# Optimization experiments

Measured on AMD Instinct MI355X. Metric: run time of the kernel, lower is better.

Reference implementation:

```python
import jax, jax.numpy as jnp
import numpy as np

B, T, C = 2, 4096, 1024
H, M, CHUNK = 16, 64, 128
D = C // H
DELTA = 1e-6


def setup_inputs() -> dict:
    key = jax.random.key(0)
    ks = jax.random.split(key, 4)
    x = jax.random.normal(ks[0], (B, T, C), dtype=jnp.float32)
    Wqkv = jax.random.normal(ks[1], (3 * C, C), dtype=jnp.float32) * 0.02
    bqkv = jnp.zeros((3 * C,), dtype=jnp.float32)
    Wout = jax.random.normal(ks[2], (C, C), dtype=jnp.float32) * 0.02
    bout = jnp.zeros((C,), dtype=jnp.float32)
    proj = jax.random.normal(ks[3], (H, D, M), dtype=jnp.float32) / np.sqrt(D)
    return {"x": x, "Wqkv": Wqkv, "bqkv": bqkv, "Wout": Wout, "bout": bout, "proj": proj}


def reference(x, Wqkv, bqkv, Wout, bout, proj):
    b, t, c = x.shape
    qkv = x @ Wqkv.T + bqkv                      # (B,T,3C)
    q, k, v = jnp.split(qkv, 3, axis=-1)
    # (B,T,C) -> (B,H,T,D)
    def to_heads(z):
        return z.reshape(b, t, H, D).transpose(0, 2, 1, 3).astype(jnp.float32)
    q, k, v = to_heads(q), to_heads(k), to_heads(v)

    nch = t // CHUNK
    # (B,H,T,D) -> (nch, B, H, Tc, D)
    def to_chunks(z):
        return z.reshape(b, H, nch, CHUNK, D).transpose(2, 0, 1, 3, 4)
    qc, kc, vc = to_chunks(q), to_chunks(k), to_chunks(v)

    mask = jnp.tril(jnp.ones((CHUNK, CHUNK), dtype=jnp.float32))

    def step(carry, inp):
        kv_state, k_state = carry                 # (B,H,M,D), (B,H,M)
        q_ch, k_ch, v_ch = inp                    # (B,H,Tc,D)
        qp = jax.nn.relu(jnp.einsum('bhtd,hdm->bhtm', q_ch, proj))
        kp = jax.nn.relu(jnp.einsum('bhtd,hdm->bhtm', k_ch, proj))
        ctx_hist = jnp.einsum('bhtm,bhmd->bhtd', qp, kv_state)
        norm_hist = jnp.einsum('bhtm,bhm->bht', qp, k_state)
        aw = jnp.einsum('bhtm,bhsm->bhts', qp, kp) * mask  # causal intra-chunk
        ctx_intra = jnp.einsum('bhts,bhsd->bhtd', aw, v_ch)
        norm_intra = aw.sum(-1)
        out = (ctx_hist + ctx_intra) / (norm_hist + norm_intra + DELTA)[..., None]
        new_kv = kv_state + jnp.einsum('bhtm,bhtd->bhmd', kp, v_ch)
        new_k = k_state + kp.sum(2)
        return (new_kv, new_k), out

    carry0 = (jnp.zeros((b, H, M, D), jnp.float32), jnp.zeros((b, H, M), jnp.float32))
    _, outs = jax.lax.scan(step, carry0, (qc, kc, vc))  # (nch,B,H,Tc,D)
    out = outs.transpose(1, 2, 0, 3, 4).reshape(b, H, t, D)  # (B,H,T,D)
    out = out.transpose(0, 2, 1, 3).reshape(b, t, c)          # (B,T,C)
    return out @ Wout.T + bout
```

## Files before the change

### kernel.cpp

```cpp
#include <hip/hip_runtime.h>
#include <stdint.h>

#define HN 16
#define DH 64
#define MF 64
#define CHK 128
#define NCH 32
#define TSEQ 4096
#define CIN 1024
#define C3 3072

typedef __attribute__((ext_vector_type(8))) short bf16x8;
typedef __attribute__((ext_vector_type(4))) float f32x4;

__device__ __forceinline__ unsigned short f2b(float f){
  union{float f;uint32_t u;} v; v.f=f;
  return (unsigned short)((v.u + 0x7fffu + ((v.u>>16)&1u))>>16);
}

#define MFMA(a,b,c) __builtin_amdgcn_mfma_f32_16x16x32_bf16(a,b,c,0,0,0)

typedef __attribute__((address_space(1))) void gbl_t;
typedef __attribute__((address_space(3))) void lds_t;
__device__ __forceinline__ void gload_lds16(const void* g, void* l){
  __builtin_amdgcn_global_load_lds((const gbl_t*)g, (lds_t*)l, 16, 0, 0);
}

__global__ __launch_bounds__(256) void cvt_kernel(const float* __restrict__ src,
                                                  unsigned short* __restrict__ dst, int n4){
  int i = blockIdx.x*256 + threadIdx.x;
  if (i >= n4) return;
  float4 v = ((const float4*)src)[i];
  uint64_t pk = (uint64_t)f2b(v.x) | ((uint64_t)f2b(v.y)<<16)
              | ((uint64_t)f2b(v.z)<<32) | ((uint64_t)f2b(v.w)<<48);
  *(uint64_t*)(dst + (size_t)i*4) = pk;
}

__global__ __launch_bounds__(256) void projt_kernel(const float* __restrict__ proj,
                                                    unsigned short* __restrict__ projT){
  int i = blockIdx.x*256 + threadIdx.x;
  if (i >= HN*DH*MF) return;
  int h = i>>12, r = i&4095, d = r>>6, m = r&63;
  projT[(h<<12) + (m<<6) + d] = f2b(proj[i]);
}

template<int OUT_BF16>
__global__ __launch_bounds__(256) void gemm_bt_kernel(
    const unsigned short* __restrict__ A, const unsigned short* __restrict__ Bt,
    const float* __restrict__ bias, void* __restrict__ Cout,
    int Mm, int Nn, int Kk)
{
  __shared__ unsigned short sA[128*32];
  __shared__ unsigned short sB[128*32];
  int tid = threadIdx.x;
  int w = tid>>6, l = tid&63, g = l>>4, r16 = l&15;
  int nb = Nn>>7;
  int brow = (blockIdx.x / nb)<<7;
  int bcol = (blockIdx.x % nb)<<7;
  int wr = w>>1, wc = w&1;
  f32x4 acc[4][4];
  #pragma unroll
  for (int m=0;m<4;m++)
    #pragma unroll
    for (int n=0;n<4;n++) acc[m][n] = (f32x4){0.f,0.f,0.f,0.f};

  int srow = tid>>2, scol = (tid&3)<<3;
  const unsigned short* Ag0 = A + (size_t)(brow+srow)*Kk + scol;
  const unsigned short* Bg0 = Bt + (size_t)(bcol+srow)*Kk + scol;
  char* lA = (char*)sA + tid*16;
  char* lB = (char*)sB + tid*16;
  size_t step64 = (size_t)64*Kk;

  for (int kk=0; kk<Kk; kk+=32){
    gload_lds16(Ag0 + kk,          lA);
    gload_lds16(Ag0 + kk + step64, lA + 4096);
    gload_lds16(Bg0 + kk,          lB);
    gload_lds16(Bg0 + kk + step64, lB + 4096);
    asm volatile("s_waitcnt vmcnt(0)" ::: "memory");
    __syncthreads();
    bf16x8 af[4], bfr[4];
    #pragma unroll
    for (int m=0;m<4;m++){
      int row = wr*64 + m*16 + r16;
      af[m] = *(const bf16x8*)((const char*)sA + row*64 + g*16);
    }
    #pragma unroll
    for (int n=0;n<4;n++){
      int row = wc*64 + n*16 + r16;
      bfr[n] = *(const bf16x8*)((const char*)sB + row*64 + g*16);
    }
    #pragma unroll
    for (int m=0;m<4;m++)
      #pragma unroll
      for (int n=0;n<4;n++)
        acc[m][n] = MFMA(af[m], bfr[n], acc[m][n]);
    __syncthreads();
  }
  #pragma unroll
  for (int m=0;m<4;m++){
    #pragma unroll
    for (int n=0;n<4;n++){
      int colg = bcol + wc*64 + n*16 + r16;
      float bv = bias[colg];
      #pragma unroll
      for (int j=0;j<4;j++){
        int rowg = brow + wr*64 + m*16 + g*4 + j;
        float v = acc[m][n][j] + bv;
        if (OUT_BF16) ((unsigned short*)Cout)[(size_t)rowg*Nn + colg] = f2b(v);
        else          ((float*)Cout)[(size_t)rowg*Nn + colg] = v;
      }
    }
  }
}

__global__ __launch_bounds__(256) void chunk_stats_kernel(
    const unsigned short* __restrict__ qkvb,
    const unsigned short* __restrict__ projT,
    float* __restrict__ Sbuf, float* __restrict__ ssum)
{
  __shared__ unsigned short s_pT[64*64];
  __shared__ unsigned short s_kpT[64*128];
  __shared__ unsigned short s_vT[64*128];
  __shared__ float s_part[256];

  int bid = blockIdx.x;
  int ch = bid&31, h = (bid>>5)&15, b = bid>>9;
  int tid = threadIdx.x, w = tid>>6, l = tid&63, g = l>>4, r16 = l&15;
  int rowbase = b*TSEQ + ch*CHK;
  const unsigned short* kg = qkvb + (size_t)rowbase*C3 + CIN   + h*DH;
  const unsigned short* vg = qkvb + (size_t)rowbase*C3 + 2*CIN + h*DH;

  {
    const unsigned short* p = projT + (h<<12);
    for (int i = tid; i < 4096; i += 256){
      int m = i>>6, d = i&63;
      *(unsigned short*)((char*)s_pT + m*128 + (((d*2) ^ ((m&7)<<4)))) = p[i];
    }
  }
  for (int i = tid; i < 1024; i += 256){
    int t = i>>3, d0 = (i&7)<<3;
    bf16x8 vv = *(const bf16x8*)(vg + (size_t)t*C3 + d0);
    #pragma unroll
    for (int j=0;j<8;j++){
      int d = d0+j;
      *(unsigned short*)((char*)s_vT + d*256 + (((t*2) ^ ((d&15)<<4)))) = (unsigned short)vv[j];
    }
  }
  __syncthreads();

  f32x4 kacc[2][4];
  #pragma unroll
  for (int tr=0;tr<2;tr++)
    #pragma unroll
    for (int nc=0;nc<4;nc++) kacc[tr][nc] = (f32x4){0.f,0.f,0.f,0.f};
  #pragma unroll
  for (int ks=0; ks<2; ks++){
    bf16x8 a[2];
    #pragma unroll
    for (int tr=0;tr<2;tr++){
      int t = w*32 + tr*16 + r16;
      a[tr] = *(const bf16x8*)(kg + (size_t)t*C3 + ks*32 + g*8);
    }
    #pragma unroll
    for (int nc=0;nc<4;nc++){
      int m = nc*16 + r16;
      bf16x8 bb = *(const bf16x8*)((const char*)s_pT + m*128 + (((ks*64 + g*16) ^ ((m&7)<<4))));
      #pragma unroll
      for (int tr=0;tr<2;tr++)
        kacc[tr][nc] = MFMA(a[tr], bb, kacc[tr][nc]);
    }
  }
  #pragma unroll
  for (int nc=0;nc<4;nc++){
    float v = 0.f;
    #pragma unroll
    for (int tr=0;tr<2;tr++)
      #pragma unroll
      for (int j=0;j<4;j++){
        float x = kacc[tr][nc][j]; x = x>0.f?x:0.f;
        v += x;
        int t = w*32 + tr*16 + g*4 + j;
        int m = nc*16 + r16;
        *(unsigned short*)((char*)s_kpT + m*256 + (((t*2) ^ ((m&15)<<4)))) = f2b(x);
      }
    v += __shfl_xor(v,16); v += __shfl_xor(v,32);
    if (g==0) s_part[w*64 + nc*16 + r16] = v;
  }
  __syncthreads();

  f32x4 sacc[4];
  #pragma unroll
  for (int dc=0;dc<4;dc++) sacc[dc] = (f32x4){0.f,0.f,0.f,0.f};
  int mrow = w*16 + r16;
  #pragma unroll
  for (int ks=0; ks<4; ks++){
    bf16x8 a = *(const bf16x8*)((const char*)s_kpT + mrow*256 + (((ks*64 + g*16) ^ ((mrow&15)<<4))));
    #pragma unroll
    for (int dc=0; dc<4; dc++){
      int d = dc*16 + r16;
      bf16x8 bb = *(const bf16x8*)((const char*)s_vT + d*256 + (((ks*64 + g*16) ^ ((d&15)<<4))));
      sacc[dc] = MFMA(a, bb, sacc[dc]);
    }
  }
  float* So = Sbuf + ((size_t)((b*HN + h)*NCH + ch))*4096;
  #pragma unroll
  for (int dc=0; dc<4; dc++)
    #pragma unroll
    for (int j=0;j<4;j++)
      So[(w*16 + g*4 + j)*64 + dc*16 + r16] = sacc[dc][j];
  if (tid < 64){
    float v = s_part[tid] + s_part[64+tid] + s_part[128+tid] + s_part[192+tid];
    ssum[((size_t)((b*HN + h)*NCH + ch))*64 + tid] = v;
  }
}

__global__ __launch_bounds__(256) void scan_kernel(
  const float* __restrict__ Sbuf, const float* __restrict__ ssum,
  float* __restrict__ kvstate, float* __restrict__ kstate)
{
  int bh = blockIdx.x, tid = threadIdx.x;
  const float4* Sp = (const float4*)(Sbuf + (size_t)bh*NCH*4096);
  float4* kvp = (float4*)(kvstate + (size_t)bh*NCH*4096);
  float4 acc[4];
  #pragma unroll
  for (int q=0;q<4;q++) acc[q] = make_float4(0.f,0.f,0.f,0.f);
  for (int c2=0; c2<NCH; c2++){
    #pragma unroll
    for (int q=0;q<4;q++){
      int idx = c2*1024 + q*256 + tid;
      float4 s = Sp[idx];
      kvp[idx] = acc[q];
      acc[q].x += s.x; acc[q].y += s.y; acc[q].z += s.z; acc[q].w += s.w;
    }
  }
  if (tid < 64){
    float a = 0.f;
    const float* sp = ssum + (size_t)bh*NCH*64;
    float* kp2 = kstate + (size_t)bh*NCH*64;
    for (int c2=0;c2<NCH;c2++){ kp2[c2*64+tid] = a; a += sp[c2*64+tid]; }
  }
}

__global__ __launch_bounds__(256) void chunk_out_kernel(
    const unsigned short* __restrict__ qkvb,
    const unsigned short* __restrict__ projT,
    const float* __restrict__ kvstate,
    const float* __restrict__ kstate,
    unsigned short* __restrict__ attnb)
{
  __shared__ unsigned short s_qp[128*64];
  __shared__ unsigned short s_kp[128*64];
  __shared__ unsigned short s_vT[64*128];
  __shared__ unsigned short s_pa[64*64];

  int bid = blockIdx.x;
  int ch = bid&31, h=(bid>>5)&15, b=bid>>9;
  int tid=threadIdx.x, w=tid>>6, l=tid&63, g=l>>4, r16=l&15;
  int rowbase = b*TSEQ + ch*CHK;
  const unsigned short* qg = qkvb + (size_t)rowbase*C3 + h*DH;
  const unsigned short* kg = qg + CIN;
  const unsigned short* vg = qg + 2*CIN;
  const float* kvg = kvstate + ((size_t)((b*HN+h)*NCH + ch))*4096;
  const float* ksg = kstate  + ((size_t)((b*HN+h)*NCH + ch))*64;

  {
    const unsigned short* p = projT + (h<<12);
    for (int i = tid; i < 4096; i += 256){
      int m = i>>6, d = i&63;
      *(unsigned short*)((char*)s_pa + m*128 + (((d*2) ^ ((m&7)<<4)))) = p[i];
    }
  }
  for (int i = tid; i < 1024; i += 256){
    int t = i>>3, d0 = (i&7)<<3;
    bf16x8 vv = *(const bf16x8*)(vg + (size_t)t*C3 + d0);
    #pragma unroll
    for (int j=0;j<8;j++){
      int d = d0+j;
      *(unsigned short*)((char*)s_vT + d*256 + (((t*2) ^ ((d&15)<<4)))) = (unsigned short)vv[j];
    }
  }
  __syncthreads();

  f32x4 qacc[2][4];
  #pragma unroll
  for (int tr=0;tr<2;tr++)
    #pragma unroll
    for (int nc=0;nc<4;nc++) qacc[tr][nc] = (f32x4){0.f,0.f,0.f,0.f};
  #pragma unroll
  for (int ks=0; ks<2; ks++){
    bf16x8 a[2];
    #pragma unroll
    for (int tr=0;tr<2;tr++){
      int t = w*32 + tr*16 + r16;
      a[tr] = *(const bf16x8*)(qg + (size_t)t*C3 + ks*32 + g*8);
    }
    #pragma unroll
    for (int nc=0;nc<4;nc++){
      int m = nc*16 + r16;
      bf16x8 bb = *(const bf16x8*)((const char*)s_pa + m*128 + (((ks*64 + g*16) ^ ((m&7)<<4))));
      #pragma unroll
      for (int tr=0;tr<2;tr++)
        qacc[tr][nc] = MFMA(a[tr], bb, qacc[tr][nc]);
    }
  }
  float nh[2][4];
  #pragma unroll
  for (int tr=0;tr<2;tr++)
    #pragma unroll
    for (int j=0;j<4;j++) nh[tr][j] = 0.f;
  #pragma unroll
  for (int nc=0;nc<4;nc++){
    float ksv = ksg[nc*16 + r16];
    #pragma unroll
    for (int tr=0;tr<2;tr++)
      #pragma unroll
      for (int j=0;j<4;j++){
        float x = qacc[tr][nc][j]; x = x>0.f?x:0.f;
        nh[tr][j] += x*ksv;
        int t = w*32 + tr*16 + g*4 + j;
        int m = nc*16 + r16;
        *(unsigned short*)((char*)s_qp + t*128 + (((m*2) ^ ((t&7)<<4)))) = f2b(x);
      }
  }
  f32x4 kacc[2][4];
  #pragma unroll
  for (int tr=0;tr<2;tr++)
    #pragma unroll
    for (int nc=0;nc<4;nc++) kacc[tr][nc] = (f32x4){0.f,0.f,0.f,0.f};
  #pragma unroll
  for (int ks=0; ks<2; ks++){
    bf16x8 a[2];
    #pragma unroll
    for (int tr=0;tr<2;tr++){
      int t = w*32 + tr*16 + r16;
      a[tr] = *(const bf16x8*)(kg + (size_t)t*C3 + ks*32 + g*8);
    }
    #pragma unroll
    for (int nc=0;nc<4;nc++){
      int m = nc*16 + r16;
      bf16x8 bb = *(const bf16x8*)((const char*)s_pa + m*128 + (((ks*64 + g*16) ^ ((m&7)<<4))));
      #pragma unroll
      for (int tr=0;tr<2;tr++)
        kacc[tr][nc] = MFMA(a[tr], bb, kacc[tr][nc]);
    }
  }
  #pragma unroll
  for (int nc=0;nc<4;nc++)
    #pragma unroll
    for (int tr=0;tr<2;tr++)
      #pragma unroll
      for (int j=0;j<4;j++){
        float x = kacc[tr][nc][j]; x = x>0.f?x:0.f;
        int t = w*32 + tr*16 + g*4 + j;
        int m = nc*16 + r16;
        *(unsigned short*)((char*)s_kp + t*128 + (((m*2) ^ ((t&7)<<4)))) = f2b(x);
      }
  __syncthreads();

  f32x4 ctx[2][4];
  float ni[2][4];
  #pragma unroll
  for (int tr=0;tr<2;tr++){
    #pragma unroll
    for (int dc=0;dc<4;dc++) ctx[tr][dc] = (f32x4){0.f,0.f,0.f,0.f};
    #pragma unroll
    for (int j=0;j<4;j++) ni[tr][j] = 0.f;
  }

  for (int sb=0; sb<4; sb++){
    f32x4 aw[2][2];
    #pragma unroll
    for (int tr=0;tr<2;tr++)
      #pragma unroll
      for (int sc=0;sc<2;sc++) aw[tr][sc] = (f32x4){0.f,0.f,0.f,0.f};
    #pragma unroll
    for (int ks=0; ks<2; ks++){
      bf16x8 a[2];
      #pragma unroll
      for (int tr=0;tr<2;tr++){
        int t = w*32 + tr*16 + r16;
        a[tr] = *(const bf16x8*)((const char*)s_qp + t*128 + (((ks*64 + g*16) ^ ((t&7)<<4))));
      }
      #pragma unroll
      for (int sc=0;sc<2;sc++){
        int s = sb*32 + sc*16 + r16;
        bf16x8 bb = *(const bf16x8*)((const char*)s_kp + s*128 + (((ks*64 + g*16) ^ ((s&7)<<4))));
        #pragma unroll
        for (int tr=0;tr<2;tr++)
          aw[tr][sc] = MFMA(a[tr], bb, aw[tr][sc]);
      }
    }
    #pragma unroll
    for (int tr=0;tr<2;tr++)
      #pragma unroll
      for (int sc=0;sc<2;sc++)
        #pragma unroll
        for (int j=0;j<4;j++){
          int t = w*32 + tr*16 + g*4 + j;
          int s = sb*32 + sc*16 + r16;
          float x = (s<=t)? aw[tr][sc][j] : 0.f;
          ni[tr][j] += x;
          int sl = sc*16 + r16;
          *(unsigned short*)((char*)s_pa + t*64 + (((sl*2) ^ ((t&3)<<4)))) = f2b(x);
        }
    __syncthreads();
    #pragma unroll
    for (int tr=0;tr<2;tr++){
      int t = w*32 + tr*16 + r16;
      bf16x8 a2 = *(const bf16x8*)((const char*)s_pa + t*64 + (((g*16) ^ ((t&3)<<4))));
      #pragma unroll
      for (int dc=0;dc<4;dc++){
        int d = dc*16 + r16;
        bf16x8 bb = *(const bf16x8*)((const char*)s_vT + d*256 + (((sb*64 + g*16) ^ ((d&15)<<4))));
        ctx[tr][dc] = MFMA(a2, bb, ctx[tr][dc]);
      }
    }
    __syncthreads();
  }

  #pragma unroll
  for (int ks=0; ks<2; ks++){
    bf16x8 a[2];
    #pragma unroll
    for (int tr=0;tr<2;tr++){
      int t = w*32 + tr*16 + r16;
      a[tr] = *(const bf16x8*)((const char*)s_qp + t*128 + (((ks*64 + g*16) ^ ((t&7)<<4))));
    }
    #pragma unroll
    for (int dc=0;dc<4;dc++){
      bf16x8 bb;
      #pragma unroll
      for (int i=0;i<8;i++)
        bb[i] = (short)f2b(kvg[(ks*32 + g*8 + i)*64 + dc*16 + r16]);
      #pragma unroll
      for (int tr=0;tr<2;tr++)
        ctx[tr][dc] = MFMA(a[tr], bb, ctx[tr][dc]);
    }
  }

  float nrm[2][4];
  #pragma unroll
  for (int tr=0;tr<2;tr++)
    #pragma unroll
    for (int j=0;j<4;j++){
      float v = nh[tr][j] + ni[tr][j];
      v += __shfl_xor(v,1); v += __shfl_xor(v,2);
      v += __shfl_xor(v,4); v += __shfl_xor(v,8);
      nrm[tr][j] = v + 1e-6f;
    }

  #pragma unroll
  for (int tr=0;tr<2;tr++)
    #pragma unroll
    for (int dc=0;dc<4;dc++)
      #pragma unroll
      for (int j=0;j<4;j++){
        int t = w*32 + tr*16 + g*4 + j;
        int d = dc*16 + r16;
        attnb[(size_t)(rowbase + t)*CIN + h*DH + d] = f2b(ctx[tr][dc][j] / nrm[tr][j]);
      }
}

extern "C" void kernel_launch(void* const* d_in, const int* in_sizes, int n_in,
                              void* d_out, int out_size, void* d_ws, size_t ws_size,
                              hipStream_t stream)
{
  const float* x    = (const float*)d_in[0];
  const float* Wqkv = (const float*)d_in[1];
  const float* bqkv = (const float*)d_in[2];
  const float* Wout = (const float*)d_in[3];
  const float* bout = (const float*)d_in[4];
  const float* proj = (const float*)d_in[5];

  char* ws = (char*)d_ws;
  unsigned short* xb     = (unsigned short*)(ws + 0);
  unsigned short* attnb  = (unsigned short*)(ws + 0);
  unsigned short* wqkvb  = (unsigned short*)(ws + 16777216);
  float*          ssum   = (float*)(ws + 16777216);
  float*          kstate = (float*)(ws + 17039360);
  unsigned short* qkvb   = (unsigned short*)(ws + 23068672);
  unsigned short* woutb  = (unsigned short*)(ws + 73400320);
  unsigned short* projTb = (unsigned short*)(ws + 75497472);
  float*          Sbuf   = (float*)(ws + 75628544);
  float*          kvstate= (float*)(ws + 92405760);

  cvt_kernel<<<8192, 256, 0, stream>>>(x, xb, 2097152);
  cvt_kernel<<<3072, 256, 0, stream>>>(Wqkv, wqkvb, 786432);
  cvt_kernel<<<1024, 256, 0, stream>>>(Wout, woutb, 262144);
  projt_kernel<<<256, 256, 0, stream>>>(proj, projTb);

  gemm_bt_kernel<1><<<1536, 256, 0, stream>>>(xb, wqkvb, bqkv, qkvb, 8192, 3072, 1024);

  chunk_stats_kernel<<<1024, 256, 0, stream>>>(qkvb, projTb, Sbuf, ssum);
  scan_kernel<<<32, 256, 0, stream>>>(Sbuf, ssum, kvstate, kstate);
  chunk_out_kernel<<<1024, 256, 0, stream>>>(qkvb, projTb, kvstate, kstate, attnb);

  gemm_bt_kernel<0><<<512, 256, 0, stream>>>(attnb, woutb, bout, d_out, 8192, 1024, 1024);
}
```

Measured before the change: 180.4 us.

## Replace GEMM with 256x256 double-buffered 8-wave pipelined kernel

Swaps the simple 128x128 single-buffer bf16 GEMM for a 256x256-tile, 512-thread kernel. It double-buffers 64-wide K slices in LDS, interleaves global-to-LDS staging across eight MFMA sub-phases, uses an XOR swizzle to avoid bank conflicts, raises wave priority around MFMA bursts, and remaps workgroups across XCDs. The goal is to hide global-load latency and improve data reuse in both projection GEMMs. In exchange it uses much more LDS per block, has fewer blocks (128 for the output GEMM, which may underfill the GPU), and needs careful vmcnt accounting, including wrap-around prefetches past the end of K.

New measurement: 191.8 us. 6.3% more time.

```diff
diff --git a/kernel.cpp b/kernel.cpp
--- a/kernel.cpp
+++ b/kernel.cpp
@@ -44,70 +44,132 @@
   projT[(h<<12) + (m<<6) + d] = f2b(proj[i]);
 }
 
-template<int OUT_BF16>
-__global__ __launch_bounds__(256) void gemm_bt_kernel(
+template<int OUT_BF16, int KK>
+__global__ __launch_bounds__(512, 2) void gemm8p_kernel(
     const unsigned short* __restrict__ A, const unsigned short* __restrict__ Bt,
     const float* __restrict__ bias, void* __restrict__ Cout,
-    int Mm, int Nn, int Kk)
+    int Nn, int nbN)
 {
-  __shared__ unsigned short sA[128*32];
-  __shared__ unsigned short sB[128*32];
+  static_assert(KK % 128 == 0, "KK multiple of 128");
+  constexpr int NT = KK / 64;
+  constexpr int NI = NT / 2;
+  static_assert((NT & (NT-1)) == 0, "NT pow2 for wrap");
+
+  __shared__ unsigned short sA[2*256*64];
+  __shared__ unsigned short sB[2*256*64];
+
   int tid = threadIdx.x;
   int w = tid>>6, l = tid&63, g = l>>4, r16 = l&15;
-  int nb = Nn>>7;
-  int brow = (blockIdx.x / nb)<<7;
-  int bcol = (blockIdx.x % nb)<<7;
-  int wr = w>>1, wc = w&1;
-  f32x4 acc[4][4];
-  #pragma unroll
-  for (int m=0;m<4;m++)
+  int wr = w>>2, wc = w&3;
+
+  int nwg = gridDim.x;
+  int qq = nwg>>3;
+  int wgid = (blockIdx.x & 7)*qq + (blockIdx.x>>3);
+  int brow = (wgid / nbN)<<8;
+  int bcol = (wgid % nbN)<<8;
+
+  int rofs = tid>>3;
+  int cofs = ((tid&7) ^ ((tid>>3)&7))<<3;
+
+  const unsigned short* Ab = A + (size_t)brow*KK;
+  const unsigned short* Bb = Bt + (size_t)bcol*KK;
+  char* sAc = (char*)sA;
+  char* sBc = (char*)sB;
+
+  f32x4 acc[8][4];
+  #pragma unroll
+  for (int m=0;m<8;m++)
     #pragma unroll
     for (int n=0;n<4;n++) acc[m][n] = (f32x4){0.f,0.f,0.f,0.f};
 
-  int srow = tid>>2, scol = (tid&3)<<3;
-  const unsigned short* Ag0 = A + (size_t)(brow+srow)*Kk + scol;
-  const unsigned short* Bg0 = Bt + (size_t)(bcol+srow)*Kk + scol;
-  char* lA = (char*)sA + tid*16;
-  char* lB = (char*)sB + tid*16;
-  size_t step64 = (size_t)64*Kk;
-
-  for (int kk=0; kk<Kk; kk+=32){
-    gload_lds16(Ag0 + kk,          lA);
-    gload_lds16(Ag0 + kk + step64, lA + 4096);
-    gload_lds16(Bg0 + kk,          lB);
-    gload_lds16(Bg0 + kk + step64, lB + 4096);
-    asm volatile("s_waitcnt vmcnt(0)" ::: "memory");
-    __syncthreads();
-    bf16x8 af[4], bfr[4];
-    #pragma unroll
-    for (int m=0;m<4;m++){
-      int row = wr*64 + m*16 + r16;
-      af[m] = *(const bf16x8*)((const char*)sA + row*64 + g*16);
-    }
-    #pragma unroll
-    for (int n=0;n<4;n++){
-      int row = wc*64 + n*16 + r16;
-      bfr[n] = *(const bf16x8*)((const char*)sB + row*64 + g*16);
-    }
-    #pragma unroll
-    for (int m=0;m<4;m++)
-      #pragma unroll
-      for (int n=0;n<4;n++)
-        acc[m][n] = MFMA(af[m], bfr[n], acc[m][n]);
-    __syncthreads();
-  }
-  #pragma unroll
-  for (int m=0;m<4;m++){
-    #pragma unroll
-    for (int n=0;n<4;n++){
-      int colg = bcol + wc*64 + n*16 + r16;
-      float bv = bias[colg];
+  auto stgA = [&](int buf, int half, int kt){
+    int r0 = half<<7;
+    const unsigned short* gp = Ab + (size_t)(r0 + rofs)*KK + (kt<<6) + cofs;
+    char* lp = sAc + (buf<<15) + (r0<<7) + (tid<<4);
+    gload_lds16(gp, lp);
+    gload_lds16(gp + (size_t)64*KK, lp + 64*128);
+  };
+  auto stgB = [&](int buf, int half, int kt){
+    int r0 = half<<7;
+    const unsigned short* gp = Bb + (size_t)(r0 + rofs)*KK + (kt<<6) + cofs;
+    char* lp = sBc + (buf<<15) + (r0<<7) + (tid<<4);
+    gload_lds16(gp, lp);
+    gload_lds16(gp + (size_t)64*KK, lp + 64*128);
+  };
+
+#define PHASE(BUF, MH, NH, STAGES, GUARD) do{                                      \
+    bf16x8 af[4][2], bfv[2][2];                                                    \
+    const char* sab = sAc + ((BUF)<<15);                                           \
+    const char* sbb = sBc + ((BUF)<<15);                                           \
+    _Pragma("unroll")                                                              \
+    for (int mf_=0; mf_<4; mf_++){                                                 \
+      int row = (MH)*128 + wr*64 + mf_*16 + r16;                                   \
+      _Pragma("unroll")                                                            \
+      for (int ks_=0; ks_<2; ks_++)                                                \
+        af[mf_][ks_] = *(const bf16x8*)(sab + row*128 + (((ks_*4+g)^(r16&7))<<4)); \
+    }                                                                              \
+    _Pragma("unroll")                                                              \
+    for (int nf_=0; nf_<2; nf_++){                                                 \
+      int row = (NH)*128 + wc*32 + nf_*16 + r16;                                   \
+      _Pragma("unroll")                                                            \
+      for (int ks_=0; ks_<2; ks_++)                                                \
+        bfv[nf_][ks_] = *(const bf16x8*)(sbb + row*128 + (((ks_*4+g)^(r16&7))<<4));\
+    }                                                                              \
+    STAGES;                                                                        \
+    GUARD;                                                                         \
+    __builtin_amdgcn_s_barrier();                                                  \
+    __builtin_amdgcn_sched_barrier(0);                                             \
+    __builtin_amdgcn_s_setprio(1);                                                 \
+    _Pragma("unroll")                                                              \
+    for (int mf_=0; mf_<4; mf_++)                                                  \
+      _Pragma("unroll")                                                            \
+      for (int nf_=0; nf_<2; nf_++)                                                \
+        _Pragma("unroll")                                                          \
+        for (int ks_=0; ks_<2; ks_++)                                              \
+          acc[(MH)*4+mf_][(NH)*2+nf_] =                                            \
+            MFMA(af[mf_][ks_], bfv[nf_][ks_], acc[(MH)*4+mf_][(NH)*2+nf_]);        \
+    __builtin_amdgcn_s_setprio(0);                                                 \
+    __builtin_amdgcn_sched_barrier(0);                                             \
+    __builtin_amdgcn_s_barrier();                                                  \
+    asm volatile("" ::: "memory");                                                 \
+  }while(0)
+
+#define VM4 asm volatile("s_waitcnt vmcnt(4)" ::: "memory")
+
+  stgA(0,0,0); stgA(0,1,0); stgB(0,0,0); stgB(0,1,0);
+  stgA(1,0,1); stgB(1,0,1);
+  VM4;
+  __builtin_amdgcn_s_barrier();
+  asm volatile("" ::: "memory");
+
+  for (int it=0; it<NI; ++it){
+    int t1 = 2*it+1;
+    int t2 = (2*it+2) & (NT-1);
+    int t3 = (2*it+3) & (NT-1);
+    PHASE(0, 0,0, { stgA(1,1,t1); stgB(1,1,t1); }, {});
+    PHASE(0, 0,1, {}, {});
+    PHASE(0, 1,0, { stgA(0,0,t2); }, {});
+    PHASE(0, 1,1, { stgB(0,0,t2); }, VM4);
+    PHASE(1, 0,0, { stgA(0,1,t2); stgB(0,1,t2); }, {});
+    PHASE(1, 0,1, {}, {});
+    PHASE(1, 1,0, { stgA(1,0,t3); }, {});
+    PHASE(1, 1,1, { stgB(1,0,t3); }, VM4);
+  }
+#undef PHASE
+#undef VM4
+
+  #pragma unroll
+  for (int n=0;n<4;n++){
+    int colg = bcol + (n>>1)*128 + wc*32 + (n&1)*16 + r16;
+    float bv = bias[colg];
+    #pragma unroll
+    for (int m=0;m<8;m++){
+      int rowg = brow + (m>>2)*128 + wr*64 + (m&3)*16 + g*4;
       #pragma unroll
       for (int j=0;j<4;j++){
-        int rowg = brow + wr*64 + m*16 + g*4 + j;
         float v = acc[m][n][j] + bv;
-        if (OUT_BF16) ((unsigned short*)Cout)[(size_t)rowg*Nn + colg] = f2b(v);
-        else          ((float*)Cout)[(size_t)rowg*Nn + colg] = v;
+        if (OUT_BF16) ((unsigned short*)Cout)[(size_t)(rowg+j)*Nn + colg] = f2b(v);
+        else          ((float*)Cout)[(size_t)(rowg+j)*Nn + colg] = v;
       }
     }
   }
@@ -489,11 +551,11 @@
   cvt_kernel<<<1024, 256, 0, stream>>>(Wout, woutb, 262144);
   projt_kernel<<<256, 256, 0, stream>>>(proj, projTb);
 
-  gemm_bt_kernel<1><<<1536, 256, 0, stream>>>(xb, wqkvb, bqkv, qkvb, 8192, 3072, 1024);
+  gemm8p_kernel<1,1024><<<384, 512, 0, stream>>>(xb, wqkvb, bqkv, qkvb, 3072, 12);
 
   chunk_stats_kernel<<<1024, 256, 0, stream>>>(qkvb, projTb, Sbuf, ssum);
   scan_kernel<<<32, 256, 0, stream>>>(Sbuf, ssum, kvstate, kstate);
   chunk_out_kernel<<<1024, 256, 0, stream>>>(qkvb, projTb, kvstate, kstate, attnb);
 
-  gemm_bt_kernel<0><<<512, 256, 0, stream>>>(attnb, woutb, bout, d_out, 8192, 1024, 1024);
-}
+  gemm8p_kernel<0,1024><<<128, 512, 0, stream>>>(attnb, woutb, bout, d_out, 1024, 4);
+}
```

## Pipeline GEMM with double-buffered swizzled LDS and direct A loads; widen scan grid

Applied to the files above, without the earlier changes.

The GEMM kernel is rewritten to use a K-step of 64, double-buffered LDS for the B operand with an XOR swizzle, A fragments loaded straight from global memory into registers one step ahead, XCD-aware remapping of workgroup ids, and raised wave priority around the MFMA block. This is meant to hide global-load latency behind compute and cut LDS bank conflicts and per-iteration barriers. Separately, the scan kernel is split four ways per batch-head so 128 blocks run instead of 32, which should improve parallelism in a latency-bound pass. The trade-off is higher register pressure from register-held A tiles and more uncoalesced A reads from global memory.

Result: slower. 224.4 us (+24.4%).

```diff
diff --git a/kernel.cpp b/kernel.cpp
--- a/kernel.cpp
+++ b/kernel.cpp
@@ -44,70 +44,102 @@
   projT[(h<<12) + (m<<6) + d] = f2b(proj[i]);
 }
 
-template<int OUT_BF16>
-__global__ __launch_bounds__(256) void gemm_bt_kernel(
+template<int OUT_BF16, int KK>
+__global__ __launch_bounds__(256, 2) void gemm_flat_kernel(
     const unsigned short* __restrict__ A, const unsigned short* __restrict__ Bt,
     const float* __restrict__ bias, void* __restrict__ Cout,
-    int Mm, int Nn, int Kk)
+    int Nn, int nbN)
 {
-  __shared__ unsigned short sA[128*32];
-  __shared__ unsigned short sB[128*32];
+  constexpr int NT = KK/64;
+  __shared__ unsigned short sB[2*128*64];
+
   int tid = threadIdx.x;
   int w = tid>>6, l = tid&63, g = l>>4, r16 = l&15;
-  int nb = Nn>>7;
-  int brow = (blockIdx.x / nb)<<7;
-  int bcol = (blockIdx.x % nb)<<7;
   int wr = w>>1, wc = w&1;
+
+  int nwg = gridDim.x, qq = nwg>>3;
+  int wgid = (blockIdx.x & 7)*qq + (blockIdx.x>>3);
+  int brow = (wgid / nbN)<<7;
+  int bcol = (wgid % nbN)<<7;
+
+  int rofs = tid>>3;
+  int cofs = ((tid&7) ^ ((tid>>3)&7))<<3;
+
+  const unsigned short* Bb = Bt + (size_t)bcol*KK;
+  char* sBc = (char*)sB;
+  const unsigned short* Arow = A + (size_t)(brow + wr*64 + r16)*KK + g*8;
+
   f32x4 acc[4][4];
   #pragma unroll
   for (int m=0;m<4;m++)
     #pragma unroll
     for (int n=0;n<4;n++) acc[m][n] = (f32x4){0.f,0.f,0.f,0.f};
 
-  int srow = tid>>2, scol = (tid&3)<<3;
-  const unsigned short* Ag0 = A + (size_t)(brow+srow)*Kk + scol;
-  const unsigned short* Bg0 = Bt + (size_t)(bcol+srow)*Kk + scol;
-  char* lA = (char*)sA + tid*16;
-  char* lB = (char*)sB + tid*16;
-  size_t step64 = (size_t)64*Kk;
-
-  for (int kk=0; kk<Kk; kk+=32){
-    gload_lds16(Ag0 + kk,          lA);
-    gload_lds16(Ag0 + kk + step64, lA + 4096);
-    gload_lds16(Bg0 + kk,          lB);
-    gload_lds16(Bg0 + kk + step64, lB + 4096);
-    asm volatile("s_waitcnt vmcnt(0)" ::: "memory");
-    __syncthreads();
-    bf16x8 af[4], bfr[4];
-    #pragma unroll
-    for (int m=0;m<4;m++){
-      int row = wr*64 + m*16 + r16;
-      af[m] = *(const bf16x8*)((const char*)sA + row*64 + g*16);
-    }
-    #pragma unroll
-    for (int n=0;n<4;n++){
-      int row = wc*64 + n*16 + r16;
-      bfr[n] = *(const bf16x8*)((const char*)sB + row*64 + g*16);
-    }
-    #pragma unroll
-    for (int m=0;m<4;m++)
-      #pragma unroll
-      for (int n=0;n<4;n++)
-        acc[m][n] = MFMA(af[m], bfr[n], acc[m][n]);
-    __syncthreads();
-  }
-  #pragma unroll
-  for (int m=0;m<4;m++){
-    #pragma unroll
-    for (int n=0;n<4;n++){
-      int colg = bcol + wc*64 + n*16 + r16;
-      float bv = bias[colg];
-      #pragma unroll
-      for (int j=0;j<4;j++){
-        int rowg = brow + wr*64 + m*16 + g*4 + j;
-        float v = acc[m][n][j] + bv;
-        if (OUT_BF16) ((unsigned short*)Cout)[(size_t)rowg*Nn + colg] = f2b(v);
-        else          ((float*)Cout)[(size_t)rowg*Nn + colg] = v;
+  auto stgB = [&](int buf, int kt){
+    const unsigned short* gp = Bb + (size_t)rofs*KK + ((size_t)kt<<6) + cofs;
+    char* lp = sBc + (buf<<14) + (tid<<4);
+    #pragma unroll
+    for (int i=0;i<4;i++)
+      gload_lds16(gp + (size_t)32*i*KK, lp + 4096*i);
+  };
+
+  bf16x8 areg[2][4][2];
+  auto aload = [&](int t, int sel){
+    #pragma unroll
+    for (int mf=0; mf<4; mf++)
+      #pragma unroll
+      for (int ks=0; ks<2; ks++)
+        areg[sel][mf][ks] = *(const bf16x8*)(Arow + (size_t)mf*16*KK + ((size_t)t<<6) + ks*32);
+  };
+
+  stgB(0, 0);
+  aload(0, 0);
+  asm volatile("s_waitcnt vmcnt(8)" ::: "memory");
+  __builtin_amdgcn_s_barrier();
+  asm volatile("" ::: "memory");
+
+  #pragma unroll 2
+  for (int t=0; t<NT; ++t){
+    int buf = t&1;
+    if (t+1 < NT) stgB(buf^1, t+1);
+    bf16x8 bfr[4][2];
+    const char* sb = sBc + (buf<<14);
+    #pragma unroll
+    for (int nf=0; nf<4; nf++){
+      int rb = wc*64 + nf*16 + r16;
+      #pragma unroll
+      for (int ks=0; ks<2; ks++)
+        bfr[nf][ks] = *(const bf16x8*)(sb + rb*128 + (((ks*4+g)^(r16&7))<<4));
+    }
+    if (t+1 < NT) aload(t+1, buf^1);
+    __builtin_amdgcn_s_setprio(1);
+    #pragma unroll
+    for (int mf=0; mf<4; mf++)
+      #pragma unroll
+      for (int nf=0; nf<4; nf++)
+        #pragma unroll
+        for (int ks=0; ks<2; ks++)
+          acc[mf][nf] = MFMA(areg[buf][mf][ks], bfr[nf][ks], acc[mf][nf]);
+    __builtin_amdgcn_s_setprio(0);
+    if (t+1 < NT){
+      asm volatile("s_waitcnt vmcnt(8)" ::: "memory");
+      __builtin_amdgcn_s_barrier();
+      asm volatile("" ::: "memory");
+    }
+  }
+
+  #pragma unroll
+  for (int nf=0; nf<4; nf++){
+    int colg = bcol + wc*64 + nf*16 + r16;
+    float bv = bias[colg];
+    #pragma unroll
+    for (int mf=0; mf<4; mf++){
+      int rowg = brow + wr*64 + mf*16 + g*4;
+      #pragma unroll
+      for (int j=0; j<4; j++){
+        float v = acc[mf][nf][j] + bv;
+        if (OUT_BF16) ((unsigned short*)Cout)[(size_t)(rowg+j)*Nn + colg] = f2b(v);
+        else          ((float*)Cout)[(size_t)(rowg+j)*Nn + colg] = v;
       }
     }
   }
@@ -218,22 +250,18 @@
   const float* __restrict__ Sbuf, const float* __restrict__ ssum,
   float* __restrict__ kvstate, float* __restrict__ kstate)
 {
-  int bh = blockIdx.x, tid = threadIdx.x;
+  int bh = blockIdx.x>>2, qd = blockIdx.x&3, tid = threadIdx.x;
   const float4* Sp = (const float4*)(Sbuf + (size_t)bh*NCH*4096);
   float4* kvp = (float4*)(kvstate + (size_t)bh*NCH*4096);
-  float4 acc[4];
-  #pragma unroll
-  for (int q=0;q<4;q++) acc[q] = make_float4(0.f,0.f,0.f,0.f);
+  int idx0 = (tid>>2)*16 + qd*4 + (tid&3);
+  float4 acc = make_float4(0.f,0.f,0.f,0.f);
   for (int c2=0; c2<NCH; c2++){
-    #pragma unroll
-    for (int q=0;q<4;q++){
-      int idx = c2*1024 + q*256 + tid;
-      float4 s = Sp[idx];
-      kvp[idx] = acc[q];
-      acc[q].x += s.x; acc[q].y += s.y; acc[q].z += s.z; acc[q].w += s.w;
-    }
-  }
-  if (tid < 64){
+    int idx = c2*1024 + idx0;
+    float4 s = Sp[idx];
+    kvp[idx] = acc;
+    acc.x += s.x; acc.y += s.y; acc.z += s.z; acc.w += s.w;
+  }
+  if (qd==0 && tid < 64){
     float a = 0.f;
     const float* sp = ssum + (size_t)bh*NCH*64;
     float* kp2 = kstate + (size_t)bh*NCH*64;
@@ -489,11 +517,11 @@
   cvt_kernel<<<1024, 256, 0, stream>>>(Wout, woutb, 262144);
   projt_kernel<<<256, 256, 0, stream>>>(proj, projTb);
 
-  gemm_bt_kernel<1><<<1536, 256, 0, stream>>>(xb, wqkvb, bqkv, qkvb, 8192, 3072, 1024);
+  gemm_flat_kernel<1,1024><<<1536, 256, 0, stream>>>(xb, wqkvb, bqkv, qkvb, 3072, 24);
 
   chunk_stats_kernel<<<1024, 256, 0, stream>>>(qkvb, projTb, Sbuf, ssum);
-  scan_kernel<<<32, 256, 0, stream>>>(Sbuf, ssum, kvstate, kstate);
+  scan_kernel<<<128, 256, 0, stream>>>(Sbuf, ssum, kvstate, kstate);
   chunk_out_kernel<<<1024, 256, 0, stream>>>(qkvb, projTb, kvstate, kstate, attnb);
 
-  gemm_bt_kernel<0><<<512, 256, 0, stream>>>(attnb, woutb, bout, d_out, 8192, 1024, 1024);
-}
+  gemm_flat_kernel<0,1024><<<512, 256, 0, stream>>>(attnb, woutb, bout, d_out, 1024, 8);
+}
```
